# Kernel optimization log

Hardware: AMD Instinct MI355X
Metric: run time of the kernel (lower is better)

## Reference

```python
import jax, jax.numpy as jnp
import numpy as np

N_EMBED = 8192
EMBED_DIM = 256


def setup_inputs() -> dict:
    key = jax.random.key(0)
    k1, k2 = jax.random.split(key)
    hidden_states = jax.random.normal(k1, (8, EMBED_DIM, 32, 32), dtype=jnp.float32)
    # original inits uniform(-1/n_e, 1/n_e); scale is irrelevant for correctness testing
    emb_weights = jax.random.uniform(
        k2, (N_EMBED, EMBED_DIM), dtype=jnp.float32,
        minval=-1.0 / N_EMBED, maxval=1.0 / N_EMBED)
    return {"hidden_states": hidden_states, "emb_weights": emb_weights}


def reference(hidden_states, emb_weights):
    # (B,C,H,W) -> (B,H,W,C)
    B, C, H, W = hidden_states.shape
    z = jnp.transpose(hidden_states, (0, 2, 3, 1))
    z_flat = z.reshape(-1, C)  # [B*H*W, C]
    # squared euclidean distance: ||z||^2 + ||e||^2 - 2 z e^T
    dist = (jnp.sum(z_flat ** 2, axis=1, keepdims=True)
            + jnp.sum(emb_weights ** 2, axis=1)
            - 2.0 * jnp.matmul(z_flat, emb_weights.T))  # [N, n_embed]
    min_encoding_indices = jnp.argmin(dist, axis=1)  # [N]
    z_q = emb_weights[min_encoding_indices].reshape(B, H, W, C)
    z_q = jnp.transpose(z_q, (0, 3, 1, 2))  # (B,C,H,W)
    min_encoding_indices = min_encoding_indices.reshape(B, -1)
    return z_q, min_encoding_indices
```

## Files before the change

kernel.cpp:

```cpp
#include <hip/hip_runtime.h>
#include <hip/hip_bf16.h>
#include <math.h>

#define C_DIM 256
#define N_EMB 8192
#define N_Z   8192
#define HWB   1024
#define MBLK  128
#define NSPLIT 4
#define SPLITC (N_EMB / NSPLIT)
#define NT    128
#define NTILES (SPLITC / NT)
#define NCHUNK (NTILES * 2)
#define CK    32
#define EPS   1.1e-3f
#define ZQ_ELEMS (N_Z * C_DIM)

typedef __attribute__((ext_vector_type(8))) short bf16x8;
typedef __attribute__((ext_vector_type(4))) float f32x4;
typedef unsigned short u16;
typedef unsigned int u32;

__device__ __forceinline__ float sqf(float x) { return __fmul_rn(x, x); }

__device__ __forceinline__ u16 f2bf(float v) {
  __hip_bfloat16 h = __float2bfloat16(v);
  u16 r; __builtin_memcpy(&r, &h, 2); return r;
}

__device__ __forceinline__ void g2l16(const u16* g, u16* l) {
  __builtin_amdgcn_global_load_lds(
      (const __attribute__((address_space(1))) unsigned int*)(const void*)g,
      (__attribute__((address_space(3))) unsigned int*)(void*)l, 16, 0, 0);
}

template <int STRIDE>
__device__ float pw_sumsq_256(const float* __restrict__ a) {
  float h[2];
#pragma unroll
  for (int hh = 0; hh < 2; ++hh) {
    const float* p = a + hh * 128 * STRIDE;
    float r0 = sqf(p[0 * STRIDE]), r1 = sqf(p[1 * STRIDE]);
    float r2 = sqf(p[2 * STRIDE]), r3 = sqf(p[3 * STRIDE]);
    float r4 = sqf(p[4 * STRIDE]), r5 = sqf(p[5 * STRIDE]);
    float r6 = sqf(p[6 * STRIDE]), r7 = sqf(p[7 * STRIDE]);
    for (int i = 8; i < 128; i += 8) {
      r0 = __fadd_rn(r0, sqf(p[(i + 0) * STRIDE]));
      r1 = __fadd_rn(r1, sqf(p[(i + 1) * STRIDE]));
      r2 = __fadd_rn(r2, sqf(p[(i + 2) * STRIDE]));
      r3 = __fadd_rn(r3, sqf(p[(i + 3) * STRIDE]));
      r4 = __fadd_rn(r4, sqf(p[(i + 4) * STRIDE]));
      r5 = __fadd_rn(r5, sqf(p[(i + 5) * STRIDE]));
      r6 = __fadd_rn(r6, sqf(p[(i + 6) * STRIDE]));
      r7 = __fadd_rn(r7, sqf(p[(i + 7) * STRIDE]));
    }
    h[hh] = __fadd_rn(__fadd_rn(__fadd_rn(r0, r1), __fadd_rn(r2, r3)),
                      __fadd_rn(__fadd_rn(r4, r5), __fadd_rn(r6, r7)));
  }
  return __fadd_rn(h[0], h[1]);
}

__device__ __forceinline__ float exact_score(const float* __restrict__ zr,
                                             const float* __restrict__ er,
                                             float z2v, float e2v) {
  float d = 0.f;
  for (int k4 = 0; k4 < 64; ++k4) {
    float4 a4 = *(const float4*)(zr + k4 * 4);
    float4 b4 = *(const float4*)(er + k4 * 4);
    d = fmaf(a4.x, b4.x, d); d = fmaf(a4.y, b4.y, d);
    d = fmaf(a4.z, b4.z, d); d = fmaf(a4.w, b4.w, d);
  }
  return __fsub_rn(__fadd_rn(z2v, e2v), __fmul_rn(2.f, d));
}

__global__ void vq_tr(const float* __restrict__ hid, float* __restrict__ zt,
                      u16* __restrict__ zbf) {
  __shared__ float tl[32][33];
  int t = threadIdx.x;
  int tx = t & 31, ty = t >> 5;
  int bb = blockIdx.x >> 8;
  int r = blockIdx.x & 255;
  int cT = r >> 5, hwT = r & 31;
#pragma unroll
  for (int p = 0; p < 4; ++p)
    tl[ty + p * 8][tx] =
        hid[((size_t)bb * C_DIM + cT * 32 + ty + p * 8) * HWB + hwT * 32 + tx];
  __syncthreads();
#pragma unroll
  for (int p = 0; p < 4; ++p) {
    float v = tl[tx][ty + p * 8];
    size_t oi = ((size_t)bb * HWB + hwT * 32 + ty + p * 8) * C_DIM + cT * 32 + tx;
    zt[oi] = v;
    zbf[oi] = f2bf(v);
  }
}

__global__ void vq_norms(const float* __restrict__ zt, const float* __restrict__ emb,
                         float* __restrict__ z2, float* __restrict__ e2,
                         u16* __restrict__ ebf) {
  int t = threadIdx.x, b = blockIdx.x;
  if (b < 32) {
    int r = b * 256 + t;
    e2[r] = pw_sumsq_256<1>(emb + (size_t)r * C_DIM);
    for (int k4 = 0; k4 < 64; ++k4) {
      float4 v = *(const float4*)(emb + (size_t)r * C_DIM + k4 * 4);
      ushort4 o;
      o.x = f2bf(v.x); o.y = f2bf(v.y); o.z = f2bf(v.z); o.w = f2bf(v.w);
      *(ushort4*)(ebf + (size_t)r * C_DIM + k4 * 4) = o;
    }
  } else {
    int n = (b - 32) * 256 + t;
    z2[n] = pw_sumsq_256<1>(zt + (size_t)n * C_DIM);
  }
}

__global__ __launch_bounds__(512, 2) void vq_filter(
    const u16* __restrict__ zbf, const u16* __restrict__ ebf,
    const float* __restrict__ zt, const float* __restrict__ emb,
    const float* __restrict__ z2g, const float* __restrict__ e2g,
    float* __restrict__ cd, int* __restrict__ ci) {
  __shared__ u16 el[2][16384];
  __shared__ float e2l[SPLITC];
  __shared__ u32 mrow[MBLK];
  __shared__ u16 rcol[MBLK * CK];
  __shared__ int rcnt[MBLK];
  __shared__ int ovfr[16];
  __shared__ int novf;
  __shared__ float wbs[8];
  __shared__ int wis[8];

  int t = threadIdx.x;
  int mb = blockIdx.x >> 2;
  int ns = blockIdx.x & 3;
  int n0z = mb * MBLK;
  int l = t & 63;
  int w = t >> 6;
  int wr = w >> 1, wc = w & 1;

  if (t < MBLK) { rcnt[t] = 0; mrow[t] = 0x7f800000u; }
  if (t == 0) novf = 0;
  for (int i = t; i < SPLITC; i += 512) e2l[i] = e2g[ns * SPLITC + i];

  bf16x8 A[2][8];
#pragma unroll
  for (int rf = 0; rf < 2; ++rf)
#pragma unroll
    for (int f = 0; f < 8; ++f)
      A[rf][f] = *(const bf16x8*)(zbf +
          (size_t)(n0z + wr * 32 + rf * 16 + (l & 15)) * C_DIM + f * 32 + ((l >> 4) << 3));

  float z2r[2][4];
#pragma unroll
  for (int rf = 0; rf < 2; ++rf)
#pragma unroll
    for (int r = 0; r < 4; ++r)
      z2r[rf][r] = z2g[n0z + wr * 32 + rf * 16 + (l >> 4) * 4 + r];

  float mpl[2][4];
#pragma unroll
  for (int rf = 0; rf < 2; ++rf)
#pragma unroll
    for (int r = 0; r < 4; ++r) mpl[rf][r] = INFINITY;

  const f32x4 vzero = {0.f, 0.f, 0.f, 0.f};
  const u16* esplit = ebf + (size_t)(ns * SPLITC) * C_DIM;

#define STAGE_E(nb_, c_)                                                      \
  {                                                                           \
    int tn_ = (c_) >> 1, kcn_ = ((c_) & 1) << 7;                              \
    const u16* bs_ = esplit + (size_t)(tn_ * NT) * C_DIM + kcn_;              \
    _Pragma("unroll")                                                         \
    for (int p_ = 0; p_ < 4; ++p_) {                                          \
      int o_ = (w * 4 + p_) * 64 + l;                                         \
      int g2_ = o_ >> 10, rr_ = (o_ >> 3) & 127, p3_ = o_ & 7;                \
      g2l16(bs_ + (size_t)rr_ * C_DIM + g2_ * 64 + ((p3_ ^ (rr_ & 7)) << 3),  \
            &el[nb_][(w * 4 + p_) * 512]);                                    \
    }                                                                         \
  }

  STAGE_E(0, 0)
  __syncthreads();

  int cur = 0;
#pragma unroll 1
  for (int pass = 0; pass < 2; ++pass) {
#pragma unroll 1
    for (int tile = 0; tile < NTILES; ++tile) {
      f32x4 acc[2][4];
#pragma unroll
      for (int rf = 0; rf < 2; ++rf)
#pragma unroll
        for (int cf = 0; cf < 4; ++cf) acc[rf][cf] = vzero;

#pragma unroll
      for (int half = 0; half < 2; ++half) {
        int c = tile * 2 + half;
        if (!(pass == 1 && c == NCHUNK - 1)) STAGE_E(cur ^ 1, (c + 1) & (NCHUNK - 1))
#pragma unroll
        for (int kf = 0; kf < 4; ++kf) {
          int g2 = kf >> 1, ks = kf & 1;
          int phys = (((ks * 4 + (l >> 4)) ^ (l & 7)) << 3);
#pragma unroll
          for (int cf = 0; cf < 4; ++cf) {
            bf16x8 bfr = *(const bf16x8*)(&el[cur][g2 * 8192 +
                           (wc * 64 + cf * 16 + (l & 15)) * 64 + phys]);
            acc[0][cf] = __builtin_amdgcn_mfma_f32_16x16x32_bf16(A[0][half * 4 + kf], bfr, acc[0][cf], 0, 0, 0);
            acc[1][cf] = __builtin_amdgcn_mfma_f32_16x16x32_bf16(A[1][half * 4 + kf], bfr, acc[1][cf], 0, 0, 0);
          }
        }
        __syncthreads();
        cur ^= 1;
      }
      float e2s[4];
#pragma unroll
      for (int cf = 0; cf < 4; ++cf)
        e2s[cf] = e2l[tile * NT + wc * 64 + cf * 16 + (l & 15)];
      if (pass == 0) {
#pragma unroll
        for (int rf = 0; rf < 2; ++rf)
#pragma unroll
          for (int r = 0; r < 4; ++r) {
            float z2v = z2r[rf][r];
            float mn = mpl[rf][r];
#pragma unroll
            for (int cf = 0; cf < 4; ++cf)
              mn = fminf(mn, fmaf(-2.f, acc[rf][cf][r], z2v + e2s[cf]));
            mpl[rf][r] = mn;
          }
      } else {
        int ne0 = ns * SPLITC + tile * NT;
#pragma unroll
        for (int rf = 0; rf < 2; ++rf)
#pragma unroll
          for (int r = 0; r < 4; ++r) {
            int rowl = wr * 32 + rf * 16 + (l >> 4) * 4 + r;
            float z2v = z2r[rf][r];
            float thr = mpl[rf][r];
#pragma unroll
            for (int cf = 0; cf < 4; ++cf) {
              float s = fmaf(-2.f, acc[rf][cf][r], z2v + e2s[cf]);
              if (s <= thr) {
                int pos = atomicAdd(&rcnt[rowl], 1);
                if (pos < CK)
                  rcol[rowl * CK + pos] = (u16)(ne0 + wc * 64 + cf * 16 + (l & 15));
              }
            }
          }
      }
    }
    if (pass == 0) {
#pragma unroll
      for (int rf = 0; rf < 2; ++rf)
#pragma unroll
        for (int r = 0; r < 4; ++r) {
          float mn = mpl[rf][r];
#pragma unroll
          for (int m = 1; m < 16; m <<= 1)
            mn = fminf(mn, __shfl_xor(mn, m, 64));
          if ((l & 15) == 0) {
            int rowl = wr * 32 + rf * 16 + (l >> 4) * 4 + r;
            atomicMin(&mrow[rowl], __float_as_uint(mn));
          }
        }
      __syncthreads();
#pragma unroll
      for (int rf = 0; rf < 2; ++rf)
#pragma unroll
        for (int r = 0; r < 4; ++r) {
          int rowl = wr * 32 + rf * 16 + (l >> 4) * 4 + r;
          mpl[rf][r] = __uint_as_float(mrow[rowl]) + EPS;
        }
    }
  }
  __syncthreads();

  {
    int row = t >> 2;
    int cnt = rcnt[row];
    float b = INFINITY; int bi = N_EMB;
    if (cnt <= CK) {
      const float* zr = zt + (size_t)(n0z + row) * C_DIM;
      float z2v = z2g[n0z + row];
      for (int p2 = (t & 3); p2 < cnt; p2 += 4) {
        int col = rcol[row * CK + p2];
        float s = exact_score(zr, emb + (size_t)col * C_DIM, z2v, e2g[col]);
        if (s < b || (s == b && col < bi)) { b = s; bi = col; }
      }
    }
#pragma unroll
    for (int m = 1; m <= 2; m <<= 1) {
      float ob = __shfl_xor(b, m, 64);
      int oi2 = __shfl_xor(bi, m, 64);
      if (ob < b || (ob == b && oi2 < bi)) { b = ob; bi = oi2; }
    }
    if ((t & 3) == 0 && cnt <= CK) {
      cd[ns * N_Z + n0z + row] = b;
      ci[ns * N_Z + n0z + row] = bi;
    }
  }

  if (t < MBLK && rcnt[t] > CK) {
    int p = atomicAdd(&novf, 1);
    if (p < 16) ovfr[p] = t;
  }
  __syncthreads();
  int no = min(novf, 16);
  for (int oi = 0; oi < no; ++oi) {
    int row = ovfr[oi];
    const float* zr = zt + (size_t)(n0z + row) * C_DIM;
    float z2v = z2g[n0z + row];
    float b = INFINITY; int bi = N_EMB;
#pragma unroll
    for (int q = 0; q < 4; ++q) {
      int col = ns * SPLITC + t * 4 + q;
      float s = exact_score(zr, emb + (size_t)col * C_DIM, z2v, e2g[col]);
      if (s < b || (s == b && col < bi)) { b = s; bi = col; }
    }
#pragma unroll
    for (int m = 1; m <= 32; m <<= 1) {
      float ob = __shfl_xor(b, m, 64);
      int oi2 = __shfl_xor(bi, m, 64);
      if (ob < b || (ob == b && oi2 < bi)) { b = ob; bi = oi2; }
    }
    if (l == 0) { wbs[w] = b; wis[w] = bi; }
    __syncthreads();
    if (t == 0) {
      for (int w2 = 1; w2 < 8; ++w2)
        if (wbs[w2] < b || (wbs[w2] == b && wis[w2] < bi)) { b = wbs[w2]; bi = wis[w2]; }
      cd[ns * N_Z + n0z + row] = b;
      ci[ns * N_Z + n0z + row] = bi;
    }
    __syncthreads();
  }
}

__global__ void vq_out(const float* __restrict__ emb, const float* __restrict__ cd,
                       const int* __restrict__ ci, float* __restrict__ out) {
  __shared__ int sidx[32];
  int t = threadIdx.x;
  int n0 = blockIdx.x * 32;
  if (t < 32) {
    int n = n0 + t;
    float b = INFINITY;
    int bi = 0;
    for (int ns = 0; ns < NSPLIT; ++ns) {
      float d = cd[ns * N_Z + n];
      int i = ci[ns * N_Z + n];
      if (d < b || (d == b && i < bi)) { b = d; bi = i; }
    }
    sidx[t] = bi;
    out[ZQ_ELEMS + n] = (float)bi;
  }
  __syncthreads();
  int bb = n0 >> 10, hw0 = n0 & 1023;
  int nl = t & 31, cg = t >> 5;
#pragma unroll
  for (int p = 0; p < 8; ++p) {
    int c0 = cg * 4 + p * 32;
    float4 v = *(const float4*)(emb + (size_t)sidx[nl] * C_DIM + c0);
    out[((size_t)bb * C_DIM + c0 + 0) * HWB + hw0 + nl] = v.x;
    out[((size_t)bb * C_DIM + c0 + 1) * HWB + hw0 + nl] = v.y;
    out[((size_t)bb * C_DIM + c0 + 2) * HWB + hw0 + nl] = v.z;
    out[((size_t)bb * C_DIM + c0 + 3) * HWB + hw0 + nl] = v.w;
  }
}

extern "C" void kernel_launch(void* const* d_in, const int* in_sizes, int n_in,
                              void* d_out, int out_size, void* d_ws, size_t ws_size,
                              hipStream_t stream) {
  const float* hid = (const float*)d_in[0];
  const float* emb = (const float*)d_in[1];
  float* out = (float*)d_out;

  float* zt = (float*)d_ws;
  float* z2 = zt + (size_t)N_Z * C_DIM;
  float* e2 = z2 + N_Z;
  float* cd = e2 + N_EMB;
  int* ci = (int*)(cd + (size_t)NSPLIT * N_Z);
  u16* zbf = (u16*)(ci + (size_t)NSPLIT * N_Z);
  u16* ebf = zbf + (size_t)N_Z * C_DIM;

  vq_tr<<<2048, 256, 0, stream>>>(hid, zt, zbf);
  vq_norms<<<64, 256, 0, stream>>>(zt, emb, z2, e2, ebf);
  vq_filter<<<(N_Z / MBLK) * NSPLIT, 512, 0, stream>>>(zbf, ebf, zt, emb, z2, e2, cd, ci);
  vq_out<<<N_Z / 32, 256, 0, stream>>>(emb, cd, ci, out);
}
```

Baseline: 219.3 us.

## Replace two-pass min/filter with single pass using running shared-memory row minimum

The filter kernel drops its two-pass scheme, where pass one computed each row's exact minimum distance and pass two recomputed all MFMA tiles to collect candidates within EPS. It now does one pass: after each tile the block atomically lowers a shared per-row running minimum and collects candidates against that current threshold. The block shrinks to 64 rows and 256 threads, with K staged in 64-wide chunks and four chunks per tile. This halves the MFMA and embedding-load work but admits more candidates early on, when the running minimum is still loose. To absorb that, CK is raised to 48 and the overflow list is unbounded, with overflow rows falling back to a full exact scan of the split.

After: 281.1 us. 28.2% more time.

```diff
diff --git a/kernel.cpp b/kernel.cpp
--- a/kernel.cpp
+++ b/kernel.cpp
@@ -6,13 +6,13 @@
 #define N_EMB 8192
 #define N_Z   8192
 #define HWB   1024
-#define MBLK  128
+#define MBLK  64
 #define NSPLIT 4
 #define SPLITC (N_EMB / NSPLIT)
 #define NT    128
 #define NTILES (SPLITC / NT)
-#define NCHUNK (NTILES * 2)
-#define CK    32
+#define NCHUNK (NTILES * 4)
+#define CK    48
 #define EPS   1.1e-3f
 #define ZQ_ELEMS (N_Z * C_DIM)
 
@@ -114,20 +114,20 @@
   }
 }
 
-__global__ __launch_bounds__(512, 2) void vq_filter(
+__global__ __launch_bounds__(256) void vq_filter(
     const u16* __restrict__ zbf, const u16* __restrict__ ebf,
     const float* __restrict__ zt, const float* __restrict__ emb,
     const float* __restrict__ z2g, const float* __restrict__ e2g,
     float* __restrict__ cd, int* __restrict__ ci) {
-  __shared__ u16 el[2][16384];
+  __shared__ u16 el[2][8192];
   __shared__ float e2l[SPLITC];
   __shared__ u32 mrow[MBLK];
   __shared__ u16 rcol[MBLK * CK];
   __shared__ int rcnt[MBLK];
-  __shared__ int ovfr[16];
+  __shared__ int ovfr[MBLK];
   __shared__ int novf;
-  __shared__ float wbs[8];
-  __shared__ int wis[8];
+  __shared__ float wbs[4];
+  __shared__ int wis[4];
 
   int t = threadIdx.x;
   int mb = blockIdx.x >> 2;
@@ -139,7 +139,7 @@
 
   if (t < MBLK) { rcnt[t] = 0; mrow[t] = 0x7f800000u; }
   if (t == 0) novf = 0;
-  for (int i = t; i < SPLITC; i += 512) e2l[i] = e2g[ns * SPLITC + i];
+  for (int i = t; i < SPLITC; i += 256) e2l[i] = e2g[ns * SPLITC + i];
 
   bf16x8 A[2][8];
 #pragma unroll
@@ -156,123 +156,87 @@
     for (int r = 0; r < 4; ++r)
       z2r[rf][r] = z2g[n0z + wr * 32 + rf * 16 + (l >> 4) * 4 + r];
 
-  float mpl[2][4];
-#pragma unroll
-  for (int rf = 0; rf < 2; ++rf)
-#pragma unroll
-    for (int r = 0; r < 4; ++r) mpl[rf][r] = INFINITY;
-
   const f32x4 vzero = {0.f, 0.f, 0.f, 0.f};
   const u16* esplit = ebf + (size_t)(ns * SPLITC) * C_DIM;
 
-#define STAGE_E(nb_, c_)                                                      \
+#define STAGE_E(nb_, tn_, kn_)                                                \
   {                                                                           \
-    int tn_ = (c_) >> 1, kcn_ = ((c_) & 1) << 7;                              \
-    const u16* bs_ = esplit + (size_t)(tn_ * NT) * C_DIM + kcn_;              \
+    const u16* bs_ = esplit + (size_t)((tn_) * NT) * C_DIM + (kn_);           \
     _Pragma("unroll")                                                         \
     for (int p_ = 0; p_ < 4; ++p_) {                                          \
       int o_ = (w * 4 + p_) * 64 + l;                                         \
-      int g2_ = o_ >> 10, rr_ = (o_ >> 3) & 127, p3_ = o_ & 7;                \
-      g2l16(bs_ + (size_t)rr_ * C_DIM + g2_ * 64 + ((p3_ ^ (rr_ & 7)) << 3),  \
+      int rr_ = o_ >> 3, p3_ = o_ & 7;                                        \
+      g2l16(bs_ + (size_t)rr_ * C_DIM + ((p3_ ^ (rr_ & 7)) << 3),             \
             &el[nb_][(w * 4 + p_) * 512]);                                    \
     }                                                                         \
   }
 
-  STAGE_E(0, 0)
+  STAGE_E(0, 0, 0)
   __syncthreads();
 
-  int cur = 0;
 #pragma unroll 1
-  for (int pass = 0; pass < 2; ++pass) {
-#pragma unroll 1
-    for (int tile = 0; tile < NTILES; ++tile) {
-      f32x4 acc[2][4];
-#pragma unroll
-      for (int rf = 0; rf < 2; ++rf)
-#pragma unroll
-        for (int cf = 0; cf < 4; ++cf) acc[rf][cf] = vzero;
-
-#pragma unroll
-      for (int half = 0; half < 2; ++half) {
-        int c = tile * 2 + half;
-        if (!(pass == 1 && c == NCHUNK - 1)) STAGE_E(cur ^ 1, (c + 1) & (NCHUNK - 1))
-#pragma unroll
-        for (int kf = 0; kf < 4; ++kf) {
-          int g2 = kf >> 1, ks = kf & 1;
-          int phys = (((ks * 4 + (l >> 4)) ^ (l & 7)) << 3);
-#pragma unroll
-          for (int cf = 0; cf < 4; ++cf) {
-            bf16x8 bfr = *(const bf16x8*)(&el[cur][g2 * 8192 +
-                           (wc * 64 + cf * 16 + (l & 15)) * 64 + phys]);
-            acc[0][cf] = __builtin_amdgcn_mfma_f32_16x16x32_bf16(A[0][half * 4 + kf], bfr, acc[0][cf], 0, 0, 0);
-            acc[1][cf] = __builtin_amdgcn_mfma_f32_16x16x32_bf16(A[1][half * 4 + kf], bfr, acc[1][cf], 0, 0, 0);
-          }
+  for (int tile = 0; tile < NTILES; ++tile) {
+    f32x4 acc[2][4];
+#pragma unroll
+    for (int rf = 0; rf < 2; ++rf)
+#pragma unroll
+      for (int cf = 0; cf < 4; ++cf) acc[rf][cf] = vzero;
+
+#pragma unroll
+    for (int kc = 0; kc < 4; ++kc) {
+      {
+        int c1 = tile * 4 + kc + 1;
+        if (c1 < NCHUNK) STAGE_E((kc + 1) & 1, c1 >> 2, ((kc + 1) & 3) * 64)
+      }
+#pragma unroll
+      for (int ks = 0; ks < 2; ++ks) {
+        int phys = (((ks * 4 + (l >> 4)) ^ (l & 7)) << 3);
+#pragma unroll
+        for (int cf = 0; cf < 4; ++cf) {
+          bf16x8 bfr = *(const bf16x8*)(&el[kc & 1][(wc * 64 + cf * 16 + (l & 15)) * 64 + phys]);
+          acc[0][cf] = __builtin_amdgcn_mfma_f32_16x16x32_bf16(A[0][kc * 2 + ks], bfr, acc[0][cf], 0, 0, 0);
+          acc[1][cf] = __builtin_amdgcn_mfma_f32_16x16x32_bf16(A[1][kc * 2 + ks], bfr, acc[1][cf], 0, 0, 0);
         }
-        __syncthreads();
-        cur ^= 1;
       }
-      float e2s[4];
-#pragma unroll
-      for (int cf = 0; cf < 4; ++cf)
-        e2s[cf] = e2l[tile * NT + wc * 64 + cf * 16 + (l & 15)];
-      if (pass == 0) {
-#pragma unroll
-        for (int rf = 0; rf < 2; ++rf)
-#pragma unroll
-          for (int r = 0; r < 4; ++r) {
-            float z2v = z2r[rf][r];
-            float mn = mpl[rf][r];
-#pragma unroll
-            for (int cf = 0; cf < 4; ++cf)
-              mn = fminf(mn, fmaf(-2.f, acc[rf][cf][r], z2v + e2s[cf]));
-            mpl[rf][r] = mn;
-          }
-      } else {
-        int ne0 = ns * SPLITC + tile * NT;
+      if (kc == 3) {
+        float e2s[4];
+#pragma unroll
+        for (int cf = 0; cf < 4; ++cf)
+          e2s[cf] = e2l[tile * NT + wc * 64 + cf * 16 + (l & 15)];
 #pragma unroll
         for (int rf = 0; rf < 2; ++rf)
 #pragma unroll
           for (int r = 0; r < 4; ++r) {
             int rowl = wr * 32 + rf * 16 + (l >> 4) * 4 + r;
             float z2v = z2r[rf][r];
-            float thr = mpl[rf][r];
+            float mn = INFINITY;
+#pragma unroll
+            for (int cf = 0; cf < 4; ++cf)
+              mn = fminf(mn, fmaf(-2.f, acc[rf][cf][r], z2v + e2s[cf]));
+            atomicMin(&mrow[rowl], __float_as_uint(mn));
+          }
+        if (tile == 0) __syncthreads();
+#pragma unroll
+        for (int rf = 0; rf < 2; ++rf)
+#pragma unroll
+          for (int r = 0; r < 4; ++r) {
+            int rowl = wr * 32 + rf * 16 + (l >> 4) * 4 + r;
+            float z2v = z2r[rf][r];
+            float thr = __uint_as_float(mrow[rowl]) + EPS;
 #pragma unroll
             for (int cf = 0; cf < 4; ++cf) {
               float s = fmaf(-2.f, acc[rf][cf][r], z2v + e2s[cf]);
               if (s <= thr) {
                 int pos = atomicAdd(&rcnt[rowl], 1);
                 if (pos < CK)
-                  rcol[rowl * CK + pos] = (u16)(ne0 + wc * 64 + cf * 16 + (l & 15));
+                  rcol[rowl * CK + pos] = (u16)(ns * SPLITC + tile * NT + wc * 64 + cf * 16 + (l & 15));
               }
             }
           }
       }
-    }
-    if (pass == 0) {
-#pragma unroll
-      for (int rf = 0; rf < 2; ++rf)
-#pragma unroll
-        for (int r = 0; r < 4; ++r) {
-          float mn = mpl[rf][r];
-#pragma unroll
-          for (int m = 1; m < 16; m <<= 1)
-            mn = fminf(mn, __shfl_xor(mn, m, 64));
-          if ((l & 15) == 0) {
-            int rowl = wr * 32 + rf * 16 + (l >> 4) * 4 + r;
-            atomicMin(&mrow[rowl], __float_as_uint(mn));
-          }
-        }
       __syncthreads();
-#pragma unroll
-      for (int rf = 0; rf < 2; ++rf)
-#pragma unroll
-        for (int r = 0; r < 4; ++r) {
-          int rowl = wr * 32 + rf * 16 + (l >> 4) * 4 + r;
-          mpl[rf][r] = __uint_as_float(mrow[rowl]) + EPS;
-        }
-    }
-  }
-  __syncthreads();
+    }
+  }
 
   {
     int row = t >> 2;
@@ -301,18 +265,18 @@
 
   if (t < MBLK && rcnt[t] > CK) {
     int p = atomicAdd(&novf, 1);
-    if (p < 16) ovfr[p] = t;
+    ovfr[p] = t;
   }
   __syncthreads();
-  int no = min(novf, 16);
+  int no = novf;
   for (int oi = 0; oi < no; ++oi) {
     int row = ovfr[oi];
     const float* zr = zt + (size_t)(n0z + row) * C_DIM;
     float z2v = z2g[n0z + row];
     float b = INFINITY; int bi = N_EMB;
 #pragma unroll
-    for (int q = 0; q < 4; ++q) {
-      int col = ns * SPLITC + t * 4 + q;
+    for (int q = 0; q < 8; ++q) {
+      int col = ns * SPLITC + t * 8 + q;
       float s = exact_score(zr, emb + (size_t)col * C_DIM, z2v, e2g[col]);
       if (s < b || (s == b && col < bi)) { b = s; bi = col; }
     }
@@ -325,7 +289,7 @@
     if (l == 0) { wbs[w] = b; wis[w] = bi; }
     __syncthreads();
     if (t == 0) {
-      for (int w2 = 1; w2 < 8; ++w2)
+      for (int w2 = 1; w2 < 4; ++w2)
         if (wbs[w2] < b || (wbs[w2] == b && wis[w2] < bi)) { b = wbs[w2]; bi = wis[w2]; }
       cd[ns * N_Z + n0z + row] = b;
       ci[ns * N_Z + n0z + row] = bi;
@@ -382,6 +346,6 @@
 
   vq_tr<<<2048, 256, 0, stream>>>(hid, zt, zbf);
   vq_norms<<<64, 256, 0, stream>>>(zt, emb, z2, e2, ebf);
-  vq_filter<<<(N_Z / MBLK) * NSPLIT, 512, 0, stream>>>(zbf, ebf, zt, emb, z2, e2, cd, ci);
+  vq_filter<<<(N_Z / MBLK) * NSPLIT, 256, 0, stream>>>(zbf, ebf, zt, emb, z2, e2, cd, ci);
   vq_out<<<N_Z / 32, 256, 0, stream>>>(emb, cd, ci, out);
 }
```
